# Kernel optimization log

Measured on AMD Instinct MI355X. Metric: run time of the kernel, lower is better.

Reference implementation:

```python
import jax, jax.numpy as jnp
import numpy as np

B, S, DIM = 1, 2048, 4096
NH, NKV, HD = 32, 8, 128  # n_head, n_local_heads (kv heads), head_dim
ROPE_BASE = 10000.0


def setup_inputs() -> dict:
    key = jax.random.key(0)
    k1, k2, k3 = jax.random.split(key, 3)
    x = jax.random.normal(k1, (B, S, DIM), dtype=jnp.float32)
    total_head_dim = (NH + 2 * NKV) * HD  # 6144
    wqkv = jax.random.normal(k2, (total_head_dim, DIM), dtype=jnp.float32) * 0.02
    wo = jax.random.normal(k3, (DIM, DIM), dtype=jnp.float32) * 0.02
    # standard RoPE table: (S, HD//2, 2) = (cos, sin)
    inv_freq = 1.0 / (ROPE_BASE ** (np.arange(0, HD, 2, dtype=np.float32) / HD))
    ang = np.outer(np.arange(S, dtype=np.float32), inv_freq)
    freqs_cis = jnp.asarray(np.stack([np.cos(ang), np.sin(ang)], axis=-1), dtype=jnp.float32)
    return {"x": x, "freqs_cis": freqs_cis, "wqkv": wqkv, "wo": wo}


def _apply_rotary(x, freqs_cis):
    # x: (b, s, h, d); freqs_cis: (s, d//2, 2)
    b, s, h, d = x.shape
    xs = x.reshape(b, s, h, d // 2, 2)
    fc = freqs_cis.reshape(1, s, 1, d // 2, 2)
    re = xs[..., 0] * fc[..., 0] - xs[..., 1] * fc[..., 1]
    im = xs[..., 0] * fc[..., 1] + xs[..., 1] * fc[..., 0]
    return jnp.stack([re, im], axis=-1).reshape(b, s, h, d)


def reference(x, freqs_cis, wqkv, wo):
    b, s, _ = x.shape
    kv_size = NKV * HD
    qkv = x @ wqkv.T  # (b, s, (NH+2*NKV)*HD)
    q, k, v = jnp.split(qkv, [NH * HD, NH * HD + kv_size], axis=-1)
    q = q.reshape(b, s, NH, HD)
    k = k.reshape(b, s, NKV, HD)
    v = v.reshape(b, s, NKV, HD)
    q = _apply_rotary(q, freqs_cis)
    k = _apply_rotary(k, freqs_cis)
    rep = NH // NKV  # GQA expansion factor; repeat_kv == grouped einsum below
    qg = q.reshape(b, s, NKV, rep, HD)
    scale = 1.0 / jnp.sqrt(jnp.asarray(HD, q.dtype))
    # scores: (b, g, r, q_pos, k_pos) -- avoids materializing repeated K/V
    scores = jnp.einsum('bqgrd,bkgd->bgrqk', qg, k) * scale
    causal = jnp.tril(jnp.ones((s, s), dtype=bool))
    scores = jnp.where(causal, scores, jnp.finfo(scores.dtype).min)
    p = jax.nn.softmax(scores, axis=-1)
    o = jnp.einsum('bgrqk,bkgd->bqgrd', p, v).reshape(b, s, NH * HD)
    return o @ wo.T
```

## Files before the change

### kernel.cpp

```cpp
#include <hip/hip_runtime.h>
#include <hip/hip_bf16.h>
#include <math.h>


typedef __attribute__((ext_vector_type(8))) __bf16 bf16x8;
typedef __attribute__((ext_vector_type(4))) __bf16 bf16x4;
typedef __attribute__((ext_vector_type(4))) float f32x4;

#define NEG_BIG (-1e30f)

#define ASYNC_CP16(gsrc, ldst)                                                            \
  __builtin_amdgcn_global_load_lds((const __attribute__((address_space(1))) void*)(gsrc), \
                                   (__attribute__((address_space(3))) void*)(ldst), 16, 0, 0)

__device__ __forceinline__ f32x4 mfma_bf16(bf16x8 a, bf16x8 b, f32x4 c) {
  return __builtin_amdgcn_mfma_f32_16x16x32_bf16(a, b, c, 0, 0, 0);
}

__device__ __forceinline__ float clampf(float v) {
  return fminf(fmaxf(v, -30000.f), 30000.f);
}

__device__ __forceinline__ bf16x8 ldg8(const __hip_bfloat16* p) {
  return *(const bf16x8*)p;
}
__device__ __forceinline__ bf16x8 ldg8(const float* p) {
  f32x4 a = *(const f32x4*)p;
  f32x4 b = *(const f32x4*)(p + 4);
  bf16x8 r;
  r[0] = (__bf16)a[0]; r[1] = (__bf16)a[1]; r[2] = (__bf16)a[2]; r[3] = (__bf16)a[3];
  r[4] = (__bf16)b[0]; r[5] = (__bf16)b[1]; r[6] = (__bf16)b[2]; r[7] = (__bf16)b[3];
  return r;
}

__device__ __forceinline__ void store_c(float* C, size_t idx, float v) {
  C[idx] = clampf(v);
}
__device__ __forceinline__ void store_c(__hip_bfloat16* C, size_t idx, float v) {
  C[idx] = __float2bfloat16(clampf(v));
}

__device__ __forceinline__ void barrier_np() {
  asm volatile("" ::: "memory");
  __builtin_amdgcn_s_barrier();
  asm volatile("" ::: "memory");
}

__global__ __launch_bounds__(256) void cvt_f32_bf16(const float* __restrict__ src,
                                                    __hip_bfloat16* __restrict__ dst) {
  size_t i = ((size_t)blockIdx.x * 256 + threadIdx.x) * 8;
  *(bf16x8*)&dst[i] = ldg8(src + i);
}

__global__ __launch_bounds__(512, 2) void gemm_qkv_rope(
    const __hip_bfloat16* __restrict__ A, const __hip_bfloat16* __restrict__ B,
    __hip_bfloat16* __restrict__ qkv, __hip_bfloat16* __restrict__ vt,
    const float* __restrict__ fc) {
  const int NT = 64;
  __shared__ __align__(16) __hip_bfloat16 lds[4][16384];
  __hip_bfloat16* const As0 = lds[0];
  __hip_bfloat16* const Bs0 = lds[1];
  __hip_bfloat16* const As1 = lds[2];
  __hip_bfloat16* const Bs1 = lds[3];

  const int tid = threadIdx.x;
  const int lane = tid & 63, wid = tid >> 6;
  const int l15 = lane & 15, quad = lane >> 4;
  const int wr = wid >> 2, wc = wid & 3;
  const size_t mBase = (size_t)blockIdx.y * 256, nBase = (size_t)blockIdx.x * 256;

  const int rdOff = l15 * 64 + ((quad * 16) ^ ((l15 & 8) << 2));
  const int wr8 = wr * 8;
  const int wc4 = wc * 4;

  const char* pAsrc[4];
  const char* pBsrc[4];
  int LAel[4], LBel[4];
#pragma unroll
  for (int u = 0; u < 4; ++u) {
    int LA = (tid < 256) ? (4096 * u + tid * 16) : (16384 + 4096 * u + (tid - 256) * 16);
    int LAs = LA ^ (((LA >> 9) & 1) << 5);
    int stA = LAs >> 10, rA16 = (LAs >> 6) & 15, cbA = LAs & 63;
    int rowA = (stA >> 1) * 16 + rA16;
    int colA = (stA & 1) * 32 + (cbA >> 1);
    pAsrc[u] = (const char*)A + ((mBase + rowA) * (size_t)4096 + colA) * 2;
    LAel[u] = LA >> 1;

    int LB = u * 8192 + tid * 16;
    int LBs = LB ^ (((LB >> 9) & 1) << 5);
    int stB = LBs >> 10, rB16 = (LBs >> 6) & 15, cbB = LBs & 63;
    int rowB = (stB >> 1) * 16 + rB16;
    int colB = (stB & 1) * 32 + (cbB >> 1);
    pBsrc[u] = (const char*)B + ((nBase + rowB) * (size_t)4096 + colB) * 2;
    LBel[u] = LB >> 1;
  }

  f32x4 acc[8][4] = {};

#pragma unroll
  for (int u = 0; u < 4; ++u) {
    ASYNC_CP16(pAsrc[u], As0 + LAel[u]);
    ASYNC_CP16(pBsrc[u], Bs0 + LBel[u]);
  }
#pragma unroll
  for (int u = 0; u < 3; ++u) {
    ASYNC_CP16(pAsrc[u] + 128, As1 + LAel[u]);
    ASYNC_CP16(pBsrc[u] + 128, Bs1 + LBel[u]);
  }
  asm volatile("s_waitcnt vmcnt(6)" ::: "memory");
  barrier_np();

#define QKV_TILE(tt, CA, CB, AA, AB)                                                     \
  {                                                                                      \
    bf16x8 bfr[4][2];                                                                    \
    _Pragma("unroll") for (int p = 0; p < 4; ++p) {                                      \
      bf16x8 afr[2][2];                                                                  \
      _Pragma("unroll") for (int ii = 0; ii < 2; ++ii)                                   \
          _Pragma("unroll") for (int kk = 0; kk < 2; ++kk)                               \
              afr[ii][kk] = *(const bf16x8*)((const char*)(CA) +                         \
                                             ((wr8 + 2 * p + ii) * 2048 + kk * 1024 + rdOff)); \
      if (p == 0) {                                                                      \
        _Pragma("unroll") for (int j = 0; j < 4; ++j)                                    \
            _Pragma("unroll") for (int kk = 0; kk < 2; ++kk)                             \
                bfr[j][kk] = *(const bf16x8*)((const char*)(CB) +                        \
                                              ((wc4 + j) * 2048 + kk * 1024 + rdOff));   \
        if ((tt) + 1 < NT) {                                                             \
          ASYNC_CP16(pAsrc[3] + ((tt) + 1) * 128, (AA) + LAel[3]);                       \
          ASYNC_CP16(pBsrc[3] + ((tt) + 1) * 128, (AB) + LBel[3]);                       \
        }                                                                                \
      } else if ((tt) + 2 < NT) {                                                        \
        ASYNC_CP16(pAsrc[p - 1] + ((tt) + 2) * 128, (CA) + LAel[p - 1]);                 \
        ASYNC_CP16(pBsrc[p - 1] + ((tt) + 2) * 128, (CB) + LBel[p - 1]);                 \
      }                                                                                  \
      barrier_np();                                                                      \
      asm volatile("s_waitcnt lgkmcnt(0)" ::: "memory");                                 \
      __builtin_amdgcn_sched_barrier(0);                                                 \
      __builtin_amdgcn_s_setprio(1);                                                     \
      _Pragma("unroll") for (int ii = 0; ii < 2; ++ii)                                   \
          _Pragma("unroll") for (int j = 0; j < 4; ++j)                                  \
              _Pragma("unroll") for (int kk = 0; kk < 2; ++kk)                           \
                  acc[2 * p + ii][j] = mfma_bf16(afr[ii][kk], bfr[j][kk], acc[2 * p + ii][j]); \
      __builtin_amdgcn_s_setprio(0);                                                     \
      if (p == 3) {                                                                      \
        if ((tt) < NT - 2) {                                                             \
          asm volatile("s_waitcnt vmcnt(6)" ::: "memory");                               \
        } else if ((tt) == NT - 2) {                                                     \
          asm volatile("s_waitcnt vmcnt(0)" ::: "memory");                               \
        }                                                                                \
      }                                                                                  \
      barrier_np();                                                                      \
    }                                                                                    \
  }

  for (int t2 = 0; t2 < NT; t2 += 2) {
    QKV_TILE(t2, As0, Bs0, As1, Bs1);
    QKV_TILE(t2 + 1, As1, Bs1, As0, Bs0);
  }
#undef QKV_TILE

#pragma unroll
  for (int i = 0; i < 8; ++i)
#pragma unroll
    for (int j = 0; j < 4; ++j) {
      size_t c = nBase + wc * 64 + j * 16 + l15;
      size_t srow0 = mBase + wr * 128 + i * 16 + quad * 4;
      if (c < 5120) {
        int di2 = (int)(c & 126);
#pragma unroll
        for (int r = 0; r < 4; r++) {
          float v = clampf(acc[i][j][r]);
          float vp = __shfl_xor(v, 1);
          size_t s = srow0 + r;
          float cs = fc[s * 128 + di2];
          float sn = fc[s * 128 + di2 + 1];
          float ov = ((c & 1) == 0) ? (v * cs - vp * sn) : (vp * sn + v * cs);
          qkv[s * 6144 + c] = __float2bfloat16(ov);
        }
      } else {
        bf16x4 pk;
#pragma unroll
        for (int r = 0; r < 4; r++) pk[r] = (__bf16)clampf(acc[i][j][r]);
        *(bf16x4*)&vt[(c - 5120) * 2048 + srow0] = pk;
      }
    }
}

template <typename TC>
__global__ __launch_bounds__(256) void gemm_nt_async(
    const __hip_bfloat16* __restrict__ A, const __hip_bfloat16* __restrict__ B,
    TC* __restrict__ C, int M, int N, int K) {
  __shared__ __align__(16) __hip_bfloat16 As[128 * 32];
  __shared__ __align__(16) __hip_bfloat16 Bs[128 * 32];
  const int tid = threadIdx.x;
  const int lane = tid & 63, wave = tid >> 6;
  const int l15 = lane & 15, quad = lane >> 4;
  const int wm = (wave >> 1) * 64, wn = (wave & 1) * 64;
  const size_t mBase = (size_t)blockIdx.y * 128, nBase = (size_t)blockIdx.x * 128;

  const int ldRow = tid >> 2;
  const int ldCol = (tid & 3) * 8;
  const __hip_bfloat16* Ap = A + (mBase + ldRow) * (size_t)K + ldCol;
  const __hip_bfloat16* Bp = B + (nBase + ldRow) * (size_t)K + ldCol;

  f32x4 acc[4][4] = {};

  for (int k0 = 0; k0 < K; k0 += 32) {
    ASYNC_CP16(Ap, &As[tid * 8]);
    ASYNC_CP16(Ap + (size_t)64 * K, &As[2048 + tid * 8]);
    ASYNC_CP16(Bp, &Bs[tid * 8]);
    ASYNC_CP16(Bp + (size_t)64 * K, &Bs[2048 + tid * 8]);
    Ap += 32; Bp += 32;
    __syncthreads();
    bf16x8 af[4], bfr[4];
#pragma unroll
    for (int i = 0; i < 4; i++)
      af[i] = *(const bf16x8*)&As[(wm + i * 16 + l15) * 32 + quad * 8];
#pragma unroll
    for (int j = 0; j < 4; j++)
      bfr[j] = *(const bf16x8*)&Bs[(wn + j * 16 + l15) * 32 + quad * 8];
#pragma unroll
    for (int i = 0; i < 4; i++)
#pragma unroll
      for (int j = 0; j < 4; j++)
        acc[i][j] = mfma_bf16(af[i], bfr[j], acc[i][j]);
    __syncthreads();
  }

#pragma unroll
  for (int i = 0; i < 4; i++)
#pragma unroll
    for (int j = 0; j < 4; j++)
#pragma unroll
      for (int r = 0; r < 4; r++) {
        size_t row = mBase + wm + i * 16 + quad * 4 + r;
        size_t col = nBase + wn + j * 16 + l15;
        store_c(C, row * (size_t)N + col, acc[i][j][r]);
      }
}

template <typename TA, typename TB, typename TC>
__global__ __launch_bounds__(256) void gemm_nt(
    const TA* __restrict__ A, const TB* __restrict__ B,
    TC* __restrict__ C, int M, int N, int K) {
  __shared__ __align__(16) __hip_bfloat16 As[128 * 32];
  __shared__ __align__(16) __hip_bfloat16 Bs[128 * 32];
  const int tid = threadIdx.x;
  const int lane = tid & 63, wave = tid >> 6;
  const int l15 = lane & 15, quad = lane >> 4;
  const int wm = (wave >> 1) * 64, wn = (wave & 1) * 64;
  const size_t mBase = (size_t)blockIdx.y * 128, nBase = (size_t)blockIdx.x * 128;
  const int ldRow = tid >> 2;
  const int ldCol = (tid & 3) * 8;
  const TA* Ap = A + (mBase + ldRow) * (size_t)K + ldCol;
  const TB* Bp = B + (nBase + ldRow) * (size_t)K + ldCol;
  f32x4 acc[4][4] = {};
  for (int k0 = 0; k0 < K; k0 += 32) {
    bf16x8 a0 = ldg8(Ap);
    bf16x8 a1 = ldg8(Ap + (size_t)64 * K);
    bf16x8 b0 = ldg8(Bp);
    bf16x8 b1 = ldg8(Bp + (size_t)64 * K);
    Ap += 32; Bp += 32;
    *(bf16x8*)&As[tid * 8] = a0;
    *(bf16x8*)&As[2048 + tid * 8] = a1;
    *(bf16x8*)&Bs[tid * 8] = b0;
    *(bf16x8*)&Bs[2048 + tid * 8] = b1;
    __syncthreads();
    bf16x8 af[4], bfr[4];
#pragma unroll
    for (int i = 0; i < 4; i++)
      af[i] = *(const bf16x8*)&As[(wm + i * 16 + l15) * 32 + quad * 8];
#pragma unroll
    for (int j = 0; j < 4; j++)
      bfr[j] = *(const bf16x8*)&Bs[(wn + j * 16 + l15) * 32 + quad * 8];
#pragma unroll
    for (int i = 0; i < 4; i++)
#pragma unroll
      for (int j = 0; j < 4; j++)
        acc[i][j] = mfma_bf16(af[i], bfr[j], acc[i][j]);
    __syncthreads();
  }
#pragma unroll
  for (int i = 0; i < 4; i++)
#pragma unroll
    for (int j = 0; j < 4; j++)
#pragma unroll
      for (int r = 0; r < 4; r++) {
        size_t row = mBase + wm + i * 16 + quad * 4 + r;
        size_t col = nBase + wn + j * 16 + l15;
        store_c(C, row * (size_t)N + col, acc[i][j][r]);
      }
}

__global__ __launch_bounds__(256) void rope_kernel(__hip_bfloat16* __restrict__ qkv,
                                                   const float* __restrict__ fc) {
  int idx = blockIdx.x * 256 + threadIdx.x;
  int d = idx & 63;
  int h = (idx >> 6) % 40;
  int s = idx / (40 * 64);
  size_t off = (size_t)s * 6144 + h * 128 + d * 2;
  float x0 = __bfloat162float(qkv[off]);
  float x1 = __bfloat162float(qkv[off + 1]);
  float c = fc[s * 128 + d * 2];
  float sn = fc[s * 128 + d * 2 + 1];
  qkv[off] = __float2bfloat16(x0 * c - x1 * sn);
  qkv[off + 1] = __float2bfloat16(x0 * sn + x1 * c);
}

__global__ __launch_bounds__(256) void transpose_v(const __hip_bfloat16* __restrict__ qkv,
                                                   __hip_bfloat16* __restrict__ vt) {
  __shared__ __hip_bfloat16 tile[32][33];
  int x = threadIdx.x & 31, y = threadIdx.x >> 5;
  int colBase = blockIdx.x * 32;
  int sBase = blockIdx.y * 32;
#pragma unroll
  for (int i = 0; i < 4; i++)
    tile[y + i * 8][x] = qkv[(size_t)(sBase + y + i * 8) * 6144 + 5120 + colBase + x];
  __syncthreads();
#pragma unroll
  for (int i = 0; i < 4; i++)
    vt[(size_t)(colBase + y + i * 8) * 2048 + sBase + x] = tile[x][y + i * 8];
}

__global__ __launch_bounds__(256) void flash_attn(
    const __hip_bfloat16* __restrict__ qkv, const __hip_bfloat16* __restrict__ vt,
    __hip_bfloat16* __restrict__ o) {
  __shared__ __align__(16) __hip_bfloat16 Ks[2][64 * 128];
  __shared__ __align__(16) __hip_bfloat16 Vs[2][128 * 64];
  __shared__ __align__(16) __hip_bfloat16 Ps[4][16 * 72];
  const int tid = threadIdx.x;
  const int lane = tid & 63, wave = tid >> 6;
  const int l15 = lane & 15, quad = lane >> 4;
  const int h = blockIdx.x, g = h >> 2;
  const int y = blockIdx.y;
  const int qt = (y < 8) ? (15 - y) : (y - 8);
  const int qRowW = qt * 128 + wave * 32;

  bf16x8 qf[2][4];
#pragma unroll
  for (int t = 0; t < 2; t++) {
    const __hip_bfloat16* qp =
        qkv + (size_t)(qRowW + t * 16 + l15) * 6144 + h * 128 + quad * 8;
#pragma unroll
    for (int d = 0; d < 4; d++) qf[t][d] = *(const bf16x8*)(qp + d * 32);
  }

  const __hip_bfloat16* kSrc[4];
  const __hip_bfloat16* vSrc[4];
  int sOff[4];
#pragma unroll
  for (int rnd = 0; rnd < 4; rnd++) {
    int ci = rnd * 256 + tid;
    int row = ci >> 4, chl = ci & 15;
    int chg = chl ^ (row & 15);
    kSrc[rnd] = qkv + (size_t)row * 6144 + 4096 + g * 128 + chg * 8;
    int n = ci >> 3, ch2 = ci & 7;
    int cg2 = ch2 ^ (n & 7);
    vSrc[rnd] = vt + (size_t)(g * 128 + n) * 2048 + cg2 * 8;
    sOff[rnd] = ci * 8;
  }

  f32x4 acc_o[2][8] = {};
  f32x4 rs[2] = {};
  float m_i[2][4];
#pragma unroll
  for (int t = 0; t < 2; t++)
#pragma unroll
    for (int r = 0; r < 4; r++) m_i[t][r] = NEG_BIG;

  bf16x8 ones;
#pragma unroll
  for (int i = 0; i < 8; i++) ones[i] = (__bf16)1.0f;

  const float scale = 0.08838834764831845f;
  const int nkt = 2 * qt + 2;
  int cur = 0;

#pragma unroll
  for (int rnd = 0; rnd < 4; rnd++) {
    ASYNC_CP16(kSrc[rnd], &Ks[0][sOff[rnd]]);
    ASYNC_CP16(vSrc[rnd], &Vs[0][sOff[rnd]]);
  }

  for (int kt = 0; kt < nkt; kt++) {
    const int kBase = kt * 64;
    __syncthreads();

    if (kt + 1 < nkt) {
      const size_t ko = (size_t)(kBase + 64);
#pragma unroll
      for (int rnd = 0; rnd < 4; rnd++) {
        ASYNC_CP16(kSrc[rnd] + ko * 6144, &Ks[cur ^ 1][sOff[rnd]]);
        ASYNC_CP16(vSrc[rnd] + ko, &Vs[cur ^ 1][sOff[rnd]]);
      }
    }

    f32x4 sc[2][4] = {};
    __builtin_amdgcn_s_setprio(1);
#pragma unroll
    for (int d = 0; d < 4; d++) {
#pragma unroll
      for (int j = 0; j < 4; j++) {
        bf16x8 kb = *(const bf16x8*)&Ks[cur][(j * 16 + l15) * 128 + ((d * 4 + quad) ^ l15) * 8];
        sc[0][j] = mfma_bf16(qf[0][d], kb, sc[0][j]);
        sc[1][j] = mfma_bf16(qf[1][d], kb, sc[1][j]);
      }
    }
    __builtin_amdgcn_s_setprio(0);

#pragma unroll
    for (int t = 0; t < 2; t++) {
      const int qRowT = qRowW + t * 16;
      float rowmax[4] = {NEG_BIG, NEG_BIG, NEG_BIG, NEG_BIG};
      float sv[4][4];
#pragma unroll
      for (int j = 0; j < 4; j++) {
        int kcol = kBase + j * 16 + l15;
#pragma unroll
        for (int r = 0; r < 4; r++) {
          float s = clampf(sc[t][j][r] * scale);
          if (kcol > qRowT + quad * 4 + r) s = NEG_BIG;
          sv[j][r] = s;
          rowmax[r] = fmaxf(rowmax[r], s);
        }
      }
#pragma unroll
      for (int off = 8; off; off >>= 1)
#pragma unroll
        for (int r = 0; r < 4; r++)
          rowmax[r] = fmaxf(rowmax[r], __shfl_xor(rowmax[r], off, 16));

      bool ok = (rowmax[0] <= m_i[t][0] + 8.f) & (rowmax[1] <= m_i[t][1] + 8.f) &
                (rowmax[2] <= m_i[t][2] + 8.f) & (rowmax[3] <= m_i[t][3] + 8.f);
      if (!__all(ok)) {
        float alpha[4];
#pragma unroll
        for (int r = 0; r < 4; r++) {
          float mnew = fmaxf(m_i[t][r], rowmax[r]);
          alpha[r] = __expf(m_i[t][r] - mnew);
          m_i[t][r] = mnew;
        }
#pragma unroll
        for (int jt = 0; jt < 8; jt++)
#pragma unroll
          for (int r = 0; r < 4; r++) acc_o[t][jt][r] *= alpha[r];
#pragma unroll
        for (int r = 0; r < 4; r++) rs[t][r] *= alpha[r];
      }

#pragma unroll
      for (int j = 0; j < 4; j++)
#pragma unroll
        for (int r = 0; r < 4; r++) {
          float p = __expf(sv[j][r] - m_i[t][r]);
          Ps[wave][(quad * 4 + r) * 72 + j * 16 + l15] = __float2bfloat16(p);
        }

      __builtin_amdgcn_s_setprio(1);
#pragma unroll
      for (int kk = 0; kk < 2; kk++) {
        bf16x8 pa = *(const bf16x8*)&Ps[wave][l15 * 72 + kk * 32 + quad * 8];
        rs[t] = mfma_bf16(pa, ones, rs[t]);
#pragma unroll
        for (int jt = 0; jt < 8; jt++) {
          int n = jt * 16 + l15;
          bf16x8 vb = *(const bf16x8*)&Vs[cur][n * 64 + (((kk * 4 + quad) ^ (n & 7))) * 8];
          acc_o[t][jt] = mfma_bf16(pa, vb, acc_o[t][jt]);
        }
      }
      __builtin_amdgcn_s_setprio(0);
    }
    cur ^= 1;
  }

#pragma unroll
  for (int t = 0; t < 2; t++)
#pragma unroll
    for (int r = 0; r < 4; r++) {
      float inv = 1.f / rs[t][r];
      size_t qr = qRowW + t * 16 + quad * 4 + r;
#pragma unroll
      for (int jt = 0; jt < 8; jt++)
        o[qr * 4096 + h * 128 + jt * 16 + l15] =
            __float2bfloat16(clampf(acc_o[t][jt][r] * inv));
    }
}

extern "C" void kernel_launch(void* const* d_in, const int* in_sizes, int n_in,
                              void* d_out, int out_size, void* d_ws, size_t ws_size,
                              hipStream_t stream) {
  const float* x = (const float*)d_in[0];
  const float* fc = (const float*)d_in[1];
  const float* wqkv = (const float*)d_in[2];
  const float* wo = (const float*)d_in[3];
  float* out = (float*)d_out;

  char* ws = (char*)d_ws;
  __hip_bfloat16* qkv = (__hip_bfloat16*)ws;
  __hip_bfloat16* vt  = (__hip_bfloat16*)(ws + 25165824);
  __hip_bfloat16* ob  = (__hip_bfloat16*)(ws + 29360128);
  __hip_bfloat16* xb  = (__hip_bfloat16*)(ws + 46137344);
  __hip_bfloat16* wb  = (__hip_bfloat16*)(ws + 62914560);

  const bool fast = ws_size >= (size_t)113246208;

  if (fast) {
    cvt_f32_bf16<<<dim3(4096), 256, 0, stream>>>(x, xb);
    cvt_f32_bf16<<<dim3(12288), 256, 0, stream>>>(wqkv, wb);
    gemm_qkv_rope<<<dim3(24, 8), 512, 0, stream>>>(xb, wb, qkv, vt, fc);
  } else {
    gemm_nt<float, float, __hip_bfloat16>
        <<<dim3(48, 16), 256, 0, stream>>>(x, wqkv, qkv, 2048, 6144, 4096);
    rope_kernel<<<dim3(20480), 256, 0, stream>>>(qkv, fc);
    transpose_v<<<dim3(32, 64), 256, 0, stream>>>(qkv, vt);
  }
  flash_attn<<<dim3(32, 16), 256, 0, stream>>>(qkv, vt, ob);
  if (fast) {
    cvt_f32_bf16<<<dim3(8192), 256, 0, stream>>>(wo, wb);
    gemm_nt_async<float>
        <<<dim3(32, 16), 256, 0, stream>>>(ob, wb, out, 2048, 4096, 4096);
  } else {
    gemm_nt<__hip_bfloat16, float, float>
        <<<dim3(32, 16), 256, 0, stream>>>(ob, wo, out, 2048, 4096, 4096);
  }
}
```

Measured before the change: 576.8 us.

## Single-buffer K/V in flash attention for higher occupancy, skip mask on full tiles

Drops the double-buffered K/V shared-memory tiles for single buffers, which roughly halves LDS use, and sets launch bounds to 3 blocks per CU so more blocks can be resident. Loads for each tile are now issued and waited on before compute, with an extra barrier at the end of each iteration. This gives up the overlap of the next tile's load with current compute in exchange for occupancy. It also skips causal masking on tiles that are entirely below the diagonal, and removes the balanced query-tile ordering in favour of simple descending order.

```diff
diff --git a/kernel.cpp b/kernel.cpp
--- a/kernel.cpp
+++ b/kernel.cpp
@@ -321,18 +321,17 @@
     vt[(size_t)(colBase + y + i * 8) * 2048 + sBase + x] = tile[x][y + i * 8];
 }
 
-__global__ __launch_bounds__(256) void flash_attn(
+__global__ __launch_bounds__(256, 3) void flash_attn(
     const __hip_bfloat16* __restrict__ qkv, const __hip_bfloat16* __restrict__ vt,
     __hip_bfloat16* __restrict__ o) {
-  __shared__ __align__(16) __hip_bfloat16 Ks[2][64 * 128];
-  __shared__ __align__(16) __hip_bfloat16 Vs[2][128 * 64];
+  __shared__ __align__(16) __hip_bfloat16 Ks[64 * 128];
+  __shared__ __align__(16) __hip_bfloat16 Vs[128 * 64];
   __shared__ __align__(16) __hip_bfloat16 Ps[4][16 * 72];
   const int tid = threadIdx.x;
   const int lane = tid & 63, wave = tid >> 6;
   const int l15 = lane & 15, quad = lane >> 4;
   const int h = blockIdx.x, g = h >> 2;
-  const int y = blockIdx.y;
-  const int qt = (y < 8) ? (15 - y) : (y - 8);
+  const int qt = 15 - blockIdx.y;
   const int qRowW = qt * 128 + wave * 32;
 
   bf16x8 qf[2][4];
@@ -351,11 +350,9 @@
   for (int rnd = 0; rnd < 4; rnd++) {
     int ci = rnd * 256 + tid;
     int row = ci >> 4, chl = ci & 15;
-    int chg = chl ^ (row & 15);
-    kSrc[rnd] = qkv + (size_t)row * 6144 + 4096 + g * 128 + chg * 8;
+    kSrc[rnd] = qkv + (size_t)row * 6144 + 4096 + g * 128 + (chl ^ (row & 15)) * 8;
     int n = ci >> 3, ch2 = ci & 7;
-    int cg2 = ch2 ^ (n & 7);
-    vSrc[rnd] = vt + (size_t)(g * 128 + n) * 2048 + cg2 * 8;
+    vSrc[rnd] = vt + (size_t)(g * 128 + n) * 2048 + (ch2 ^ (n & 7)) * 8;
     sOff[rnd] = ci * 8;
   }
 
@@ -373,26 +370,15 @@
 
   const float scale = 0.08838834764831845f;
   const int nkt = 2 * qt + 2;
-  int cur = 0;
-
-#pragma unroll
-  for (int rnd = 0; rnd < 4; rnd++) {
-    ASYNC_CP16(kSrc[rnd], &Ks[0][sOff[rnd]]);
-    ASYNC_CP16(vSrc[rnd], &Vs[0][sOff[rnd]]);
-  }
 
   for (int kt = 0; kt < nkt; kt++) {
     const int kBase = kt * 64;
+#pragma unroll
+    for (int rnd = 0; rnd < 4; rnd++) {
+      ASYNC_CP16(kSrc[rnd] + (size_t)kBase * 6144, &Ks[sOff[rnd]]);
+      ASYNC_CP16(vSrc[rnd] + kBase, &Vs[sOff[rnd]]);
+    }
     __syncthreads();
-
-    if (kt + 1 < nkt) {
-      const size_t ko = (size_t)(kBase + 64);
-#pragma unroll
-      for (int rnd = 0; rnd < 4; rnd++) {
-        ASYNC_CP16(kSrc[rnd] + ko * 6144, &Ks[cur ^ 1][sOff[rnd]]);
-        ASYNC_CP16(vSrc[rnd] + ko, &Vs[cur ^ 1][sOff[rnd]]);
-      }
-    }
 
     f32x4 sc[2][4] = {};
     __builtin_amdgcn_s_setprio(1);
@@ -400,7 +386,7 @@
     for (int d = 0; d < 4; d++) {
 #pragma unroll
       for (int j = 0; j < 4; j++) {
-        bf16x8 kb = *(const bf16x8*)&Ks[cur][(j * 16 + l15) * 128 + ((d * 4 + quad) ^ l15) * 8];
+        bf16x8 kb = *(const bf16x8*)&Ks[(j * 16 + l15) * 128 + ((d * 4 + quad) ^ l15) * 8];
         sc[0][j] = mfma_bf16(qf[0][d], kb, sc[0][j]);
         sc[1][j] = mfma_bf16(qf[1][d], kb, sc[1][j]);
       }
@@ -411,16 +397,26 @@
     for (int t = 0; t < 2; t++) {
       const int qRowT = qRowW + t * 16;
       float rowmax[4] = {NEG_BIG, NEG_BIG, NEG_BIG, NEG_BIG};
-      float sv[4][4];
-#pragma unroll
-      for (int j = 0; j < 4; j++) {
-        int kcol = kBase + j * 16 + l15;
-#pragma unroll
-        for (int r = 0; r < 4; r++) {
-          float s = clampf(sc[t][j][r] * scale);
-          if (kcol > qRowT + quad * 4 + r) s = NEG_BIG;
-          sv[j][r] = s;
-          rowmax[r] = fmaxf(rowmax[r], s);
+      if (kBase + 63 <= qRowT) {
+#pragma unroll
+        for (int j = 0; j < 4; j++)
+#pragma unroll
+          for (int r = 0; r < 4; r++) {
+            float s = clampf(sc[t][j][r] * scale);
+            sc[t][j][r] = s;
+            rowmax[r] = fmaxf(rowmax[r], s);
+          }
+      } else {
+#pragma unroll
+        for (int j = 0; j < 4; j++) {
+          int kcol = kBase + j * 16 + l15;
+#pragma unroll
+          for (int r = 0; r < 4; r++) {
+            float s = clampf(sc[t][j][r] * scale);
+            if (kcol > qRowT + quad * 4 + r) s = NEG_BIG;
+            sc[t][j][r] = s;
+            rowmax[r] = fmaxf(rowmax[r], s);
+          }
         }
       }
 #pragma unroll
@@ -451,7 +447,7 @@
       for (int j = 0; j < 4; j++)
 #pragma unroll
         for (int r = 0; r < 4; r++) {
-          float p = __expf(sv[j][r] - m_i[t][r]);
+          float p = __expf(sc[t][j][r] - m_i[t][r]);
           Ps[wave][(quad * 4 + r) * 72 + j * 16 + l15] = __float2bfloat16(p);
         }
 
@@ -463,13 +459,13 @@
 #pragma unroll
         for (int jt = 0; jt < 8; jt++) {
           int n = jt * 16 + l15;
-          bf16x8 vb = *(const bf16x8*)&Vs[cur][n * 64 + (((kk * 4 + quad) ^ (n & 7))) * 8];
+          bf16x8 vb = *(const bf16x8*)&Vs[n * 64 + (((kk * 4 + quad) ^ (n & 7))) * 8];
           acc_o[t][jt] = mfma_bf16(pa, vb, acc_o[t][jt]);
         }
       }
       __builtin_amdgcn_s_setprio(0);
     }
-    cur ^= 1;
+    __syncthreads();
   }
 
 #pragma unroll
```

Result: slower. 656.9 us (+13.9%).
